# Kernel tuning notes

Hardware: AMD Instinct MI355X
Metric: run time of the kernel (lower is better)

The kernel has to match this reference:

```python
import jax, jax.numpy as jnp
import numpy as np

N, E, F_IN, HID, HEADS, G = 50000, 800000, 128, 32, 8, 64
NEG_SLOPE = 0.2  # PyG GATConv default leaky_relu slope


def gat_conv(x, src, dst, W, att_src, att_dst, bias, heads, out_ch):
    """PyG-style GATConv (concat=True, self-loops already included in src/dst)."""
    n = x.shape[0]
    h = (x @ W).reshape(n, heads, out_ch)            # [N,H,C]
    a_src = jnp.sum(h * att_src, axis=-1)            # [N,H]
    a_dst = jnp.sum(h * att_dst, axis=-1)            # [N,H]
    e = jax.nn.leaky_relu(a_src[src] + a_dst[dst], NEG_SLOPE)  # [Et,H]
    # segment softmax over incoming edges of each destination node
    m = jax.ops.segment_max(e, dst, num_segments=n)
    e = jnp.exp(e - m[dst])
    denom = jax.ops.segment_sum(e, dst, num_segments=n)
    alpha = e / (denom[dst] + 1e-16)                 # [Et,H]
    msg = h[src] * alpha[:, :, None]                 # [Et,H,C]
    out = jax.ops.segment_sum(msg, dst, num_segments=n)
    return out.reshape(n, heads * out_ch) + bias


def setup_inputs() -> dict:
    key = jax.random.key(0)
    ks = jax.random.split(key, 16)
    x = jax.random.normal(ks[0], (N, F_IN), dtype=jnp.float32)
    edge_index = jax.random.randint(ks[1], (2, E), 0, N, dtype=jnp.int64)
    batch = jnp.sort(jax.random.randint(ks[2], (N,), 0, G, dtype=jnp.int64))
    s = 0.05
    params = dict(
        W1=jax.random.normal(ks[3], (F_IN, HEADS * HID), jnp.float32) * s,
        att_src1=jax.random.normal(ks[4], (1, HEADS, HID), jnp.float32) * s,
        att_dst1=jax.random.normal(ks[5], (1, HEADS, HID), jnp.float32) * s,
        b1=jnp.zeros((HEADS * HID,), jnp.float32),
        W2=jax.random.normal(ks[6], (HEADS * HID, HID), jnp.float32) * s,
        att_src2=jax.random.normal(ks[7], (1, 1, HID), jnp.float32) * s,
        att_dst2=jax.random.normal(ks[8], (1, 1, HID), jnp.float32) * s,
        b2=jnp.zeros((HID,), jnp.float32),
        Wo=jax.random.normal(ks[9], (HID, 1), jnp.float32) * s,
        bo=jnp.zeros((1,), jnp.float32),
    )
    return dict(x=x, edge_index=edge_index, batch=batch, **params)


def reference(x, edge_index, batch, W1, att_src1, att_dst1, b1,
              W2, att_src2, att_dst2, b2, Wo, bo):
    # add self loops (PyG GATConv default add_self_loops=True)
    loop = jnp.arange(N, dtype=edge_index.dtype)
    src = jnp.concatenate([edge_index[0], loop])
    dst = jnp.concatenate([edge_index[1], loop])

    h = jax.nn.elu(gat_conv(x, src, dst, W1, att_src1, att_dst1, b1, HEADS, HID))
    # dropout p=0.2 is identity in eval mode
    h = jax.nn.elu(gat_conv(h, src, dst, W2, att_src2, att_dst2, b2, 1, HID))

    # global mean pool over graphs
    sums = jax.ops.segment_sum(h, batch, num_segments=G)          # [G,HID]
    cnts = jax.ops.segment_sum(jnp.ones((N,), h.dtype), batch, num_segments=G)
    pooled = sums / jnp.maximum(cnts, 1.0)[:, None]

    return jax.nn.sigmoid(pooled @ Wo + bo)                        # [G,1]
```

## Files before the change

kernel.cpp:

```cpp
#include <hip/hip_runtime.h>
#include <hip/hip_bf16.h>
#include <math.h>

#define NN 50000
#define NE 800000
#define ET (NE + NN)
#define FIN 128
#define HEADS 8
#define HID 32
#define C1 (HEADS * HID)
#define NG 64
#define NEG 0.2f

#define EPB 4096
#define NBKT 782
#define CAP 2048

typedef __attribute__((ext_vector_type(8))) unsigned short ushort8_t;
typedef __attribute__((ext_vector_type(4))) unsigned short ushort4_t;
typedef __attribute__((ext_vector_type(2))) float float2_t;
typedef __attribute__((ext_vector_type(8))) short bf16x8;
typedef __attribute__((ext_vector_type(4))) float f32x4;

__device__ __forceinline__ float lrelu(float v) { return v > 0.f ? v : NEG * v; }
__device__ __forceinline__ float elu1(float v)  { return v > 0.f ? v : expm1f(v); }
__device__ __forceinline__ unsigned short f2bf(float f) {
    __hip_bfloat16 b = __float2bfloat16(f);
    return *reinterpret_cast<unsigned short*>(&b);
}
__device__ __forceinline__ float bf2f(unsigned short u) {
    return __uint_as_float(((unsigned)u) << 16);
}
__device__ __forceinline__ void dec_fma16(uint4 r, float e, float2_t* acc) {
    float2_t ev = {e, e};
    acc[0] += ev * __builtin_amdgcn_cvt_pk_f32_fp8((int)r.x, false);
    acc[1] += ev * __builtin_amdgcn_cvt_pk_f32_fp8((int)r.x, true);
    acc[2] += ev * __builtin_amdgcn_cvt_pk_f32_fp8((int)r.y, false);
    acc[3] += ev * __builtin_amdgcn_cvt_pk_f32_fp8((int)r.y, true);
    acc[4] += ev * __builtin_amdgcn_cvt_pk_f32_fp8((int)r.z, false);
    acc[5] += ev * __builtin_amdgcn_cvt_pk_f32_fp8((int)r.z, true);
    acc[6] += ev * __builtin_amdgcn_cvt_pk_f32_fp8((int)r.w, false);
    acc[7] += ev * __builtin_amdgcn_cvt_pk_f32_fp8((int)r.w, true);
}

__global__ __launch_bounds__(256) void bkt_scatter_kernel(const int* __restrict__ ei,
                                                          int* __restrict__ bcur,
                                                          unsigned* __restrict__ bkt) {
    __shared__ unsigned ep[EPB];
    __shared__ int lh[NBKT];
    int t = threadIdx.x;
    int base = blockIdx.x * EPB;
    int nloc = ET - base; if (nloc > EPB) nloc = EPB;
    for (int i = t; i < NBKT; i += 256) lh[i] = 0;
    __syncthreads();
    for (int k = t; k < nloc; k += 256) {
        int i = base + k;
        int s, d;
        if (i < NE) { s = ei[i]; d = ei[NE + i]; }
        else        { s = i - NE; d = s; }
        ep[k] = (unsigned)s | ((unsigned)(d & 63) << 16) | ((unsigned)(d >> 6) << 22);
        atomicAdd(&lh[d >> 6], 1);
    }
    __syncthreads();
    for (int i = t; i < NBKT; i += 256) {
        int c = lh[i];
        lh[i] = c ? atomicAdd(&bcur[i], c) : 0;
    }
    __syncthreads();
    for (int k = t; k < nloc; k += 256) {
        unsigned v = ep[k];
        int b = (int)(v >> 22);
        int pos = atomicAdd(&lh[b], 1);
        if (pos < CAP) bkt[(size_t)b * CAP + pos] = v & 0x3FFFFFu;
    }
}

__global__ __launch_bounds__(256) void csr_kernel(const unsigned* __restrict__ bkt,
                                                  const int* __restrict__ bcur,
                                                  int* __restrict__ rowptr,
                                                  int* __restrict__ ssrc) {
    __shared__ int nb[64];
    __shared__ int nc[64];
    __shared__ int red[256];
    int b = blockIdx.x, t = threadIdx.x;
    int partial = 0;
    for (int i = t; i < b; i += 256) partial += bcur[i];
    red[t] = partial;
    if (t < 64) nc[t] = 0;
    __syncthreads();
    if (t < 128) red[t] += red[t + 128];
    __syncthreads();
    if (t < 64) {
        int v = red[t] + red[t + 64];
        #pragma unroll
        for (int off = 32; off; off >>= 1) v += __shfl_down(v, off, 64);
        if (t == 0) red[0] = v;
    }
    __syncthreads();
    int gbase = red[0];
    int cnt = bcur[b]; if (cnt > CAP) cnt = CAP;
    const unsigned* e = bkt + (size_t)b * CAP;
    for (int k = t; k < cnt; k += 256)
        atomicAdd(&nc[e[k] >> 16], 1);
    __syncthreads();
    if (t < 64) {
        int v = nc[t];
        int inc = v;
        #pragma unroll
        for (int off = 1; off < 64; off <<= 1) {
            int u = __shfl_up(inc, off, 64);
            if (t >= off) inc += u;
        }
        int start = gbase + inc - v;
        nb[t] = start;
        int node = b * 64 + t;
        if (node < NN) rowptr[node] = start;
    }
    if (b == NBKT - 1 && t == 0) rowptr[NN] = gbase + cnt;
    __syncthreads();
    for (int k = t; k < cnt; k += 256) {
        unsigned v = e[k];
        int pos = atomicAdd(&nb[v >> 16], 1);
        ssrc[pos] = (int)(v & 0xFFFFu);
    }
}

__global__ __launch_bounds__(256) void cvt_w_kernel(const float* __restrict__ W1,
                                                    const float* __restrict__ W2,
                                                    unsigned short* __restrict__ w1swz,
                                                    unsigned short* __restrict__ w2swz) {
    int bid = blockIdx.x;
    if (bid < 16) {
        int t = bid * 256 + threadIdx.x;
        int fid = t >> 6, lane = t & 63;
        int tnt = fid >> 2, ks = fid & 3;
        int n = tnt * 16 + (lane & 15);
        int k0 = ks * 32 + (lane >> 4) * 8;
        ushort8_t o;
        #pragma unroll
        for (int j = 0; j < 8; ++j) o[j] = f2bf(W1[(k0 + j) * C1 + n]);
        *(ushort8_t*)&w1swz[(size_t)(fid * 64 + lane) * 8] = o;
    } else {
        int t = (bid - 16) * 256 + threadIdx.x;
        int fid = t >> 6, lane = t & 63;
        int nt = fid >> 3, ks = fid & 7;
        int n = nt * 16 + (lane & 15);
        int k0 = ks * 32 + (lane >> 4) * 8;
        ushort8_t o;
        #pragma unroll
        for (int j = 0; j < 8; ++j) o[j] = f2bf(W2[(k0 + j) * HID + n]);
        *(ushort8_t*)&w2swz[(size_t)(fid * 64 + lane) * 8] = o;
    }
}

__global__ __launch_bounds__(256) void gemm1_kernel(
        const float* __restrict__ x, const unsigned short* __restrict__ w1swz,
        const float* __restrict__ attS, const float* __restrict__ attD,
        unsigned char* __restrict__ h1f8, float* __restrict__ aS, float* __restrict__ aD) {
    __shared__ float lds[4 * 16 * 132];
    int t = threadIdx.x, w = t >> 6, lane = t & 63;
    int mh = w & 1, nh = w >> 1;
    int m0 = blockIdx.x * 64 + mh * 32;
    int l15 = lane & 15, l4 = lane >> 4;

    f32x4 acc[2][8];
    #pragma unroll
    for (int mt = 0; mt < 2; ++mt)
        #pragma unroll
        for (int nt = 0; nt < 8; ++nt)
            acc[mt][nt] = (f32x4){0.f, 0.f, 0.f, 0.f};

    int ra = m0 + l15;       if (ra >= NN) ra = NN - 1;
    int rb = m0 + 16 + l15;  if (rb >= NN) rb = NN - 1;
    const float* a0p = x + (size_t)ra * FIN + l4 * 8;
    const float* a1p = x + (size_t)rb * FIN + l4 * 8;

    #pragma unroll
    for (int ks = 0; ks < 4; ++ks) {
        float4 f00 = *(const float4*)(a0p + ks * 32);
        float4 f01 = *(const float4*)(a0p + ks * 32 + 4);
        float4 f10 = *(const float4*)(a1p + ks * 32);
        float4 f11 = *(const float4*)(a1p + ks * 32 + 4);
        bf16x8 af0, af1;
        af0[0] = (short)f2bf(f00.x); af0[1] = (short)f2bf(f00.y);
        af0[2] = (short)f2bf(f00.z); af0[3] = (short)f2bf(f00.w);
        af0[4] = (short)f2bf(f01.x); af0[5] = (short)f2bf(f01.y);
        af0[6] = (short)f2bf(f01.z); af0[7] = (short)f2bf(f01.w);
        af1[0] = (short)f2bf(f10.x); af1[1] = (short)f2bf(f10.y);
        af1[2] = (short)f2bf(f10.z); af1[3] = (short)f2bf(f10.w);
        af1[4] = (short)f2bf(f11.x); af1[5] = (short)f2bf(f11.y);
        af1[6] = (short)f2bf(f11.z); af1[7] = (short)f2bf(f11.w);
        #pragma unroll
        for (int nt = 0; nt < 8; ++nt) {
            bf16x8 bf = *(const bf16x8*)&w1swz[(size_t)(((nh * 8 + nt) * 4 + ks) * 64 + lane) * 8];
            acc[0][nt] = __builtin_amdgcn_mfma_f32_16x16x32_bf16(af0, bf, acc[0][nt], 0, 0, 0);
            acc[1][nt] = __builtin_amdgcn_mfma_f32_16x16x32_bf16(af1, bf, acc[1][nt], 0, 0, 0);
        }
    }

    float* wl = lds + w * 16 * 132;
    #pragma unroll
    for (int mt = 0; mt < 2; ++mt) {
        __syncthreads();
        #pragma unroll
        for (int nt = 0; nt < 8; ++nt)
            #pragma unroll
            for (int r = 0; r < 4; ++r)
                wl[(l4 * 4 + r) * 132 + nt * 16 + l15] = acc[mt][nt][r];
        __syncthreads();
        int row_g = m0 + mt * 16 + l15;
        int cch = l4;
        float v[32];
        #pragma unroll
        for (int i = 0; i < 8; ++i) {
            float4 f = *(const float4*)&wl[l15 * 132 + cch * 32 + i * 4];
            v[i * 4 + 0] = f.x; v[i * 4 + 1] = f.y; v[i * 4 + 2] = f.z; v[i * 4 + 3] = f.w;
        }
        if (row_g < NN) {
            unsigned pk[8];
            #pragma unroll
            for (int i = 0; i < 8; ++i) {
                int p = __builtin_amdgcn_cvt_pk_fp8_f32(v[i * 4 + 0], v[i * 4 + 1], 0, false);
                p = __builtin_amdgcn_cvt_pk_fp8_f32(v[i * 4 + 2], v[i * 4 + 3], p, true);
                pk[i] = (unsigned)p;
            }
            size_t base = (size_t)row_g * C1 + nh * 128 + cch * 32;
            *(uint4*)&h1f8[base]      = make_uint4(pk[0], pk[1], pk[2], pk[3]);
            *(uint4*)&h1f8[base + 16] = make_uint4(pk[4], pk[5], pk[6], pk[7]);
            int h = nh * 4 + cch;
            float ps = 0.f, pd = 0.f;
            #pragma unroll
            for (int i = 0; i < 32; ++i) {
                ps += v[i] * attS[h * 32 + i];
                pd += v[i] * attD[h * 32 + i];
            }
            aS[row_g * HEADS + h] = ps;
            aD[row_g * HEADS + h] = pd;
        }
    }
}

__global__ __launch_bounds__(256) void agg1_kernel(
        const int* __restrict__ rowptr, const int* __restrict__ ssrc,
        const float* __restrict__ aS, const float* __restrict__ aD,
        const unsigned char* __restrict__ h1f8, const float* __restrict__ b1,
        unsigned short* __restrict__ z1b) {
    int d = (blockIdx.x * 256 + threadIdx.x) >> 6;
    int lane = threadIdx.x & 63;
    if (d >= NN) return;
    int start = rowptr[d], end = rowptr[d + 1];
    int q = lane >> 4, sl = lane & 15;
    int h = sl >> 1;
    float adh = aD[d * HEADS + h];
    float2_t acc[8];
    #pragma unroll
    for (int i = 0; i < 8; ++i) acc[i] = (float2_t){0.f, 0.f};
    float den = 0.f;
    int j = start + q;
    for (; j + 12 < end; j += 16) {
        int s0 = ssrc[j], s1 = ssrc[j + 4], s2 = ssrc[j + 8], s3 = ssrc[j + 12];
        uint4 r0 = *(const uint4*)&h1f8[(size_t)s0 * C1 + sl * 16];
        uint4 r1 = *(const uint4*)&h1f8[(size_t)s1 * C1 + sl * 16];
        uint4 r2 = *(const uint4*)&h1f8[(size_t)s2 * C1 + sl * 16];
        uint4 r3 = *(const uint4*)&h1f8[(size_t)s3 * C1 + sl * 16];
        float e0 = __expf(lrelu(aS[s0 * HEADS + h] + adh));
        float e1 = __expf(lrelu(aS[s1 * HEADS + h] + adh));
        float e2 = __expf(lrelu(aS[s2 * HEADS + h] + adh));
        float e3 = __expf(lrelu(aS[s3 * HEADS + h] + adh));
        den += e0 + e1 + e2 + e3;
        dec_fma16(r0, e0, acc);
        dec_fma16(r1, e1, acc);
        dec_fma16(r2, e2, acc);
        dec_fma16(r3, e3, acc);
    }
    for (; j < end; j += 4) {
        int s = ssrc[j];
        uint4 r = *(const uint4*)&h1f8[(size_t)s * C1 + sl * 16];
        float e = __expf(lrelu(aS[s * HEADS + h] + adh));
        den += e;
        dec_fma16(r, e, acc);
    }
    den += __shfl_xor(den, 16, 64);
    den += __shfl_xor(den, 32, 64);
    #pragma unroll
    for (int i = 0; i < 8; ++i) {
        acc[i].x += __shfl_xor(acc[i].x, 16, 64);
        acc[i].y += __shfl_xor(acc[i].y, 16, 64);
        acc[i].x += __shfl_xor(acc[i].x, 32, 64);
        acc[i].y += __shfl_xor(acc[i].y, 32, 64);
    }
    float invd = 1.f / (den + 1e-16f);
    int cb = sl * 16 + q * 4;
    float4 bb = *(const float4*)&b1[cb];
    ushort4_t o;
    o[0] = f2bf(elu1(acc[q * 2 + 0].x * invd + bb.x));
    o[1] = f2bf(elu1(acc[q * 2 + 0].y * invd + bb.y));
    o[2] = f2bf(elu1(acc[q * 2 + 1].x * invd + bb.z));
    o[3] = f2bf(elu1(acc[q * 2 + 1].y * invd + bb.w));
    *(ushort4_t*)&z1b[(size_t)d * C1 + cb] = o;
}

__global__ __launch_bounds__(256) void gemm2_kernel(
        const unsigned short* __restrict__ z1b, const unsigned short* __restrict__ w2swz,
        const float* __restrict__ attS, const float* __restrict__ attD,
        unsigned short* __restrict__ h2b, float* __restrict__ aS2, float* __restrict__ aD2) {
    __shared__ float lds[4 * 16 * 36];
    int t = threadIdx.x, w = t >> 6, lane = t & 63;
    int m0 = blockIdx.x * 64 + w * 16;
    int l15 = lane & 15, l4 = lane >> 4;

    f32x4 acc[2];
    acc[0] = (f32x4){0.f, 0.f, 0.f, 0.f};
    acc[1] = (f32x4){0.f, 0.f, 0.f, 0.f};

    int ra = m0 + l15; if (ra >= NN) ra = NN - 1;
    const unsigned short* ap = z1b + (size_t)ra * C1 + l4 * 8;

    #pragma unroll
    for (int ks = 0; ks < 8; ++ks) {
        bf16x8 af = *(const bf16x8*)(ap + ks * 32);
        #pragma unroll
        for (int nt = 0; nt < 2; ++nt) {
            bf16x8 bf = *(const bf16x8*)&w2swz[(size_t)((nt * 8 + ks) * 64 + lane) * 8];
            acc[nt] = __builtin_amdgcn_mfma_f32_16x16x32_bf16(af, bf, acc[nt], 0, 0, 0);
        }
    }
    float* wl = lds + w * 16 * 36;
    #pragma unroll
    for (int nt = 0; nt < 2; ++nt)
        #pragma unroll
        for (int r = 0; r < 4; ++r)
            wl[(l4 * 4 + r) * 36 + nt * 16 + l15] = acc[nt][r];
    __syncthreads();
    int row_g = m0 + l15;
    float v[8];
    {
        float4 f0 = *(const float4*)&wl[l15 * 36 + l4 * 8];
        float4 f1 = *(const float4*)&wl[l15 * 36 + l4 * 8 + 4];
        v[0] = f0.x; v[1] = f0.y; v[2] = f0.z; v[3] = f0.w;
        v[4] = f1.x; v[5] = f1.y; v[6] = f1.z; v[7] = f1.w;
    }
    float ps = 0.f, pd = 0.f;
    #pragma unroll
    for (int i = 0; i < 8; ++i) {
        ps += v[i] * attS[l4 * 8 + i];
        pd += v[i] * attD[l4 * 8 + i];
    }
    ps += __shfl_xor(ps, 16, 64); ps += __shfl_xor(ps, 32, 64);
    pd += __shfl_xor(pd, 16, 64); pd += __shfl_xor(pd, 32, 64);
    if (row_g < NN) {
        ushort8_t o;
        #pragma unroll
        for (int i = 0; i < 8; ++i) o[i] = f2bf(v[i]);
        *(ushort8_t*)&h2b[(size_t)row_g * HID + l4 * 8] = o;
        if (l4 == 0) { aS2[row_g] = ps; aD2[row_g] = pd; }
    }
}

__global__ __launch_bounds__(256) void agg2_kernel(
        const int* __restrict__ rowptr, const int* __restrict__ ssrc,
        const float* __restrict__ aS, const float* __restrict__ aD,
        const unsigned short* __restrict__ h2b, const float* __restrict__ b2,
        float* __restrict__ z2) {
    int d = (blockIdx.x * 256 + threadIdx.x) >> 6;
    int lane = threadIdx.x & 63;
    if (d >= NN) return;
    int start = rowptr[d], end = rowptr[d + 1];
    int q = lane >> 4, sl = lane & 15;
    float adv = aD[d];
    float2_t a = {0.f, 0.f};
    float den = 0.f;
    int j = start + q;
    for (; j + 12 < end; j += 16) {
        int s0 = ssrc[j], s1 = ssrc[j + 4], s2 = ssrc[j + 8], s3 = ssrc[j + 12];
        unsigned r0 = *(const unsigned*)&h2b[(size_t)s0 * HID + sl * 2];
        unsigned r1 = *(const unsigned*)&h2b[(size_t)s1 * HID + sl * 2];
        unsigned r2 = *(const unsigned*)&h2b[(size_t)s2 * HID + sl * 2];
        unsigned r3 = *(const unsigned*)&h2b[(size_t)s3 * HID + sl * 2];
        float e0 = __expf(lrelu(aS[s0] + adv));
        float e1 = __expf(lrelu(aS[s1] + adv));
        float e2 = __expf(lrelu(aS[s2] + adv));
        float e3 = __expf(lrelu(aS[s3] + adv));
        den += e0 + e1 + e2 + e3;
        a += (float2_t){e0, e0} * (float2_t){bf2f((unsigned short)(r0 & 0xffff)), bf2f((unsigned short)(r0 >> 16))};
        a += (float2_t){e1, e1} * (float2_t){bf2f((unsigned short)(r1 & 0xffff)), bf2f((unsigned short)(r1 >> 16))};
        a += (float2_t){e2, e2} * (float2_t){bf2f((unsigned short)(r2 & 0xffff)), bf2f((unsigned short)(r2 >> 16))};
        a += (float2_t){e3, e3} * (float2_t){bf2f((unsigned short)(r3 & 0xffff)), bf2f((unsigned short)(r3 >> 16))};
    }
    for (; j < end; j += 4) {
        int s = ssrc[j];
        unsigned r = *(const unsigned*)&h2b[(size_t)s * HID + sl * 2];
        float e = __expf(lrelu(aS[s] + adv));
        den += e;
        a += (float2_t){e, e} * (float2_t){bf2f((unsigned short)(r & 0xffff)), bf2f((unsigned short)(r >> 16))};
    }
    den += __shfl_xor(den, 16, 64);
    den += __shfl_xor(den, 32, 64);
    a.x += __shfl_xor(a.x, 16, 64); a.x += __shfl_xor(a.x, 32, 64);
    a.y += __shfl_xor(a.y, 16, 64); a.y += __shfl_xor(a.y, 32, 64);
    if (q == 0) {
        float invd = 1.f / (den + 1e-16f);
        float2 o;
        o.x = elu1(a.x * invd + b2[sl * 2]);
        o.y = elu1(a.y * invd + b2[sl * 2 + 1]);
        *(float2*)&z2[(size_t)d * HID + sl * 2] = o;
    }
}

__global__ __launch_bounds__(256) void pool_kernel(
        const float* __restrict__ z2, const int* __restrict__ batch,
        const float* __restrict__ Wo, const float* __restrict__ bo,
        float* __restrict__ out) {
    __shared__ float sm[256];
    int g = blockIdx.x;
    int t = threadIdx.x;
    int lo = 0, hi = NN;
    while (lo < hi) { int m = (lo + hi) >> 1; if (batch[m] < g) lo = m + 1; else hi = m; }
    int start = lo;
    hi = NN;
    while (lo < hi) { int m = (lo + hi) >> 1; if (batch[m] < g + 1) lo = m + 1; else hi = m; }
    int end = lo;
    int c = t & 31, r = t >> 5;
    float acc = 0.f;
    for (int n = start + r; n < end; n += 8)
        acc += z2[(size_t)n * HID + c];
    sm[t] = acc;
    __syncthreads();
    if (t < 32) {
        float s = 0.f;
        #pragma unroll
        for (int i = 0; i < 8; ++i) s += sm[t + 32 * i];
        float cntf = fmaxf((float)(end - start), 1.f);
        float part = (s / cntf) * Wo[t];
        #pragma unroll
        for (int off = 16; off; off >>= 1) part += __shfl_xor(part, off, 32);
        if (t == 0) out[g] = 1.f / (1.f + __expf(-(part + bo[0])));
    }
}

extern "C" void kernel_launch(void* const* d_in, const int* in_sizes, int n_in,
                              void* d_out, int out_size, void* d_ws, size_t ws_size,
                              hipStream_t stream) {
    const float* x     = (const float*)d_in[0];
    const int*   ei    = (const int*)d_in[1];
    const int*   batch = (const int*)d_in[2];
    const float* W1    = (const float*)d_in[3];
    const float* attS1 = (const float*)d_in[4];
    const float* attD1 = (const float*)d_in[5];
    const float* b1    = (const float*)d_in[6];
    const float* W2    = (const float*)d_in[7];
    const float* attS2 = (const float*)d_in[8];
    const float* attD2 = (const float*)d_in[9];
    const float* b2    = (const float*)d_in[10];
    const float* Wo    = (const float*)d_in[11];
    const float* bo    = (const float*)d_in[12];
    float* out = (float*)d_out;

    char* p = (char*)d_ws;
    auto alloc = [&](size_t bytes) {
        char* r = p;
        p += (bytes + 255) & ~(size_t)255;
        return (void*)r;
    };
    unsigned char*  h1f8  = (unsigned char*)alloc((size_t)NN * C1);
    unsigned short* w1swz = (unsigned short*)alloc((size_t)FIN * C1 * 2);
    unsigned short* w2swz = (unsigned short*)alloc((size_t)C1 * HID * 2);
    unsigned short* z1b   = (unsigned short*)alloc((size_t)NN * C1 * 2);
    unsigned short* h2b   = (unsigned short*)alloc((size_t)NN * HID * 2);
    float* aS1    = (float*)alloc((size_t)NN * HEADS * 4);
    float* aD1    = (float*)alloc((size_t)NN * HEADS * 4);
    float* z2     = (float*)alloc((size_t)NN * HID * 4);
    float* aS2    = (float*)alloc((size_t)NN * 4);
    float* aD2    = (float*)alloc((size_t)NN * 4);
    int*   rowptr = (int*)alloc((size_t)(NN + 1) * 4);
    int*   ssrc   = (int*)alloc((size_t)ET * 4);
    unsigned* bkt = (unsigned*)alloc((size_t)NBKT * CAP * 4);
    int*   bcur   = (int*)alloc((size_t)NBKT * 4);

    hipMemsetAsync(bcur, 0, (size_t)NBKT * 4, stream);
    bkt_scatter_kernel<<<(ET + EPB - 1) / EPB, 256, 0, stream>>>(ei, bcur, bkt);
    csr_kernel<<<NBKT, 256, 0, stream>>>(bkt, bcur, rowptr, ssrc);
    cvt_w_kernel<<<20, 256, 0, stream>>>(W1, W2, w1swz, w2swz);
    gemm1_kernel<<<(NN + 63) / 64, 256, 0, stream>>>(x, w1swz, attS1, attD1, h1f8, aS1, aD1);
    agg1_kernel<<<(NN * 64) / 256, 256, 0, stream>>>(rowptr, ssrc, aS1, aD1, h1f8, b1, z1b);
    gemm2_kernel<<<(NN + 63) / 64, 256, 0, stream>>>(z1b, w2swz, attS2, attD2, h2b, aS2, aD2);
    agg2_kernel<<<(NN * 64 + 255) / 256, 256, 0, stream>>>(rowptr, ssrc, aS2, aD2, h2b, b2, z2);
    pool_kernel<<<NG, 256, 0, stream>>>(z2, batch, Wo, bo, out);
}
```

Measured before the change: 271.8 us.

## Fuse edge bucket scatter with first GEMM in one launch; shrink aggregation unroll

The bucket scatter and the layer-1 GEMM are independent, so they now run as one launch with block-index dispatch over a shared LDS buffer. The weight conversion moves ahead of that launch. This removes one launch and lets the memory-bound atomic scatter overlap with the GEMM blocks. Separately, both aggregation kernels unroll by 2 edges per lane instead of 4, which lowers register pressure but also exposes less memory-level parallelism per thread.

New measurement: 246.6 us. -9.2%, faster.

```diff
diff --git a/kernel.cpp b/kernel.cpp
--- a/kernel.cpp
+++ b/kernel.cpp
@@ -13,6 +13,8 @@
 #define NEG 0.2f
 
 #define EPB 4096
+#define NB_SCAT 208
+#define NB_G1 782
 #define NBKT 782
 #define CAP 2048
 
@@ -43,13 +45,12 @@
     acc[7] += ev * __builtin_amdgcn_cvt_pk_f32_fp8((int)r.w, true);
 }
 
-__global__ __launch_bounds__(256) void bkt_scatter_kernel(const int* __restrict__ ei,
-                                                          int* __restrict__ bcur,
-                                                          unsigned* __restrict__ bkt) {
-    __shared__ unsigned ep[EPB];
-    __shared__ int lh[NBKT];
+__device__ void bkt_scatter_body(char* smem, const int* __restrict__ ei,
+                                 int* __restrict__ bcur, unsigned* __restrict__ bkt, int bid) {
+    unsigned* ep = (unsigned*)smem;
+    int* lh = (int*)(smem + EPB * 4);
     int t = threadIdx.x;
-    int base = blockIdx.x * EPB;
+    int base = bid * EPB;
     int nloc = ET - base; if (nloc > EPB) nloc = EPB;
     for (int i = t; i < NBKT; i += 256) lh[i] = 0;
     __syncthreads();
@@ -75,92 +76,15 @@
     }
 }
 
-__global__ __launch_bounds__(256) void csr_kernel(const unsigned* __restrict__ bkt,
-                                                  const int* __restrict__ bcur,
-                                                  int* __restrict__ rowptr,
-                                                  int* __restrict__ ssrc) {
-    __shared__ int nb[64];
-    __shared__ int nc[64];
-    __shared__ int red[256];
-    int b = blockIdx.x, t = threadIdx.x;
-    int partial = 0;
-    for (int i = t; i < b; i += 256) partial += bcur[i];
-    red[t] = partial;
-    if (t < 64) nc[t] = 0;
-    __syncthreads();
-    if (t < 128) red[t] += red[t + 128];
-    __syncthreads();
-    if (t < 64) {
-        int v = red[t] + red[t + 64];
-        #pragma unroll
-        for (int off = 32; off; off >>= 1) v += __shfl_down(v, off, 64);
-        if (t == 0) red[0] = v;
-    }
-    __syncthreads();
-    int gbase = red[0];
-    int cnt = bcur[b]; if (cnt > CAP) cnt = CAP;
-    const unsigned* e = bkt + (size_t)b * CAP;
-    for (int k = t; k < cnt; k += 256)
-        atomicAdd(&nc[e[k] >> 16], 1);
-    __syncthreads();
-    if (t < 64) {
-        int v = nc[t];
-        int inc = v;
-        #pragma unroll
-        for (int off = 1; off < 64; off <<= 1) {
-            int u = __shfl_up(inc, off, 64);
-            if (t >= off) inc += u;
-        }
-        int start = gbase + inc - v;
-        nb[t] = start;
-        int node = b * 64 + t;
-        if (node < NN) rowptr[node] = start;
-    }
-    if (b == NBKT - 1 && t == 0) rowptr[NN] = gbase + cnt;
-    __syncthreads();
-    for (int k = t; k < cnt; k += 256) {
-        unsigned v = e[k];
-        int pos = atomicAdd(&nb[v >> 16], 1);
-        ssrc[pos] = (int)(v & 0xFFFFu);
-    }
-}
-
-__global__ __launch_bounds__(256) void cvt_w_kernel(const float* __restrict__ W1,
-                                                    const float* __restrict__ W2,
-                                                    unsigned short* __restrict__ w1swz,
-                                                    unsigned short* __restrict__ w2swz) {
-    int bid = blockIdx.x;
-    if (bid < 16) {
-        int t = bid * 256 + threadIdx.x;
-        int fid = t >> 6, lane = t & 63;
-        int tnt = fid >> 2, ks = fid & 3;
-        int n = tnt * 16 + (lane & 15);
-        int k0 = ks * 32 + (lane >> 4) * 8;
-        ushort8_t o;
-        #pragma unroll
-        for (int j = 0; j < 8; ++j) o[j] = f2bf(W1[(k0 + j) * C1 + n]);
-        *(ushort8_t*)&w1swz[(size_t)(fid * 64 + lane) * 8] = o;
-    } else {
-        int t = (bid - 16) * 256 + threadIdx.x;
-        int fid = t >> 6, lane = t & 63;
-        int nt = fid >> 3, ks = fid & 7;
-        int n = nt * 16 + (lane & 15);
-        int k0 = ks * 32 + (lane >> 4) * 8;
-        ushort8_t o;
-        #pragma unroll
-        for (int j = 0; j < 8; ++j) o[j] = f2bf(W2[(k0 + j) * HID + n]);
-        *(ushort8_t*)&w2swz[(size_t)(fid * 64 + lane) * 8] = o;
-    }
-}
-
-__global__ __launch_bounds__(256) void gemm1_kernel(
-        const float* __restrict__ x, const unsigned short* __restrict__ w1swz,
-        const float* __restrict__ attS, const float* __restrict__ attD,
-        unsigned char* __restrict__ h1f8, float* __restrict__ aS, float* __restrict__ aD) {
-    __shared__ float lds[4 * 16 * 132];
+__device__ void gemm1_body(char* smem, const float* __restrict__ x,
+                           const unsigned short* __restrict__ w1swz,
+                           const float* __restrict__ attS, const float* __restrict__ attD,
+                           unsigned char* __restrict__ h1f8, float* __restrict__ aS,
+                           float* __restrict__ aD, int bid) {
+    float* lds = (float*)smem;
     int t = threadIdx.x, w = t >> 6, lane = t & 63;
     int mh = w & 1, nh = w >> 1;
-    int m0 = blockIdx.x * 64 + mh * 32;
+    int m0 = bid * 64 + mh * 32;
     int l15 = lane & 15, l4 = lane >> 4;
 
     f32x4 acc[2][8];
@@ -240,6 +164,96 @@
     }
 }
 
+__global__ __launch_bounds__(256) void fused_front_kernel(
+        const int* __restrict__ ei, int* __restrict__ bcur, unsigned* __restrict__ bkt,
+        const float* __restrict__ x, const unsigned short* __restrict__ w1swz,
+        const float* __restrict__ attS, const float* __restrict__ attD,
+        unsigned char* __restrict__ h1f8, float* __restrict__ aS, float* __restrict__ aD) {
+    __shared__ __align__(16) char smem[33792];
+    if (blockIdx.x < NB_SCAT)
+        bkt_scatter_body(smem, ei, bcur, bkt, blockIdx.x);
+    else
+        gemm1_body(smem, x, w1swz, attS, attD, h1f8, aS, aD, blockIdx.x - NB_SCAT);
+}
+
+__global__ __launch_bounds__(256) void csr_kernel(const unsigned* __restrict__ bkt,
+                                                  const int* __restrict__ bcur,
+                                                  int* __restrict__ rowptr,
+                                                  int* __restrict__ ssrc) {
+    __shared__ int nb[64];
+    __shared__ int nc[64];
+    __shared__ int red[256];
+    int b = blockIdx.x, t = threadIdx.x;
+    int partial = 0;
+    for (int i = t; i < b; i += 256) partial += bcur[i];
+    red[t] = partial;
+    if (t < 64) nc[t] = 0;
+    __syncthreads();
+    if (t < 128) red[t] += red[t + 128];
+    __syncthreads();
+    if (t < 64) {
+        int v = red[t] + red[t + 64];
+        #pragma unroll
+        for (int off = 32; off; off >>= 1) v += __shfl_down(v, off, 64);
+        if (t == 0) red[0] = v;
+    }
+    __syncthreads();
+    int gbase = red[0];
+    int cnt = bcur[b]; if (cnt > CAP) cnt = CAP;
+    const unsigned* e = bkt + (size_t)b * CAP;
+    for (int k = t; k < cnt; k += 256)
+        atomicAdd(&nc[e[k] >> 16], 1);
+    __syncthreads();
+    if (t < 64) {
+        int v = nc[t];
+        int inc = v;
+        #pragma unroll
+        for (int off = 1; off < 64; off <<= 1) {
+            int u = __shfl_up(inc, off, 64);
+            if (t >= off) inc += u;
+        }
+        int start = gbase + inc - v;
+        nb[t] = start;
+        int node = b * 64 + t;
+        if (node < NN) rowptr[node] = start;
+    }
+    if (b == NBKT - 1 && t == 0) rowptr[NN] = gbase + cnt;
+    __syncthreads();
+    for (int k = t; k < cnt; k += 256) {
+        unsigned v = e[k];
+        int pos = atomicAdd(&nb[v >> 16], 1);
+        ssrc[pos] = (int)(v & 0xFFFFu);
+    }
+}
+
+__global__ __launch_bounds__(256) void cvt_w_kernel(const float* __restrict__ W1,
+                                                    const float* __restrict__ W2,
+                                                    unsigned short* __restrict__ w1swz,
+                                                    unsigned short* __restrict__ w2swz) {
+    int bid = blockIdx.x;
+    if (bid < 16) {
+        int t = bid * 256 + threadIdx.x;
+        int fid = t >> 6, lane = t & 63;
+        int tnt = fid >> 2, ks = fid & 3;
+        int n = tnt * 16 + (lane & 15);
+        int k0 = ks * 32 + (lane >> 4) * 8;
+        ushort8_t o;
+        #pragma unroll
+        for (int j = 0; j < 8; ++j) o[j] = f2bf(W1[(k0 + j) * C1 + n]);
+        *(ushort8_t*)&w1swz[(size_t)(fid * 64 + lane) * 8] = o;
+    } else {
+        int t = (bid - 16) * 256 + threadIdx.x;
+        int fid = t >> 6, lane = t & 63;
+        int nt = fid >> 3, ks = fid & 7;
+        int n = nt * 16 + (lane & 15);
+        int k0 = ks * 32 + (lane >> 4) * 8;
+        ushort8_t o;
+        #pragma unroll
+        for (int j = 0; j < 8; ++j) o[j] = f2bf(W2[(k0 + j) * HID + n]);
+        *(ushort8_t*)&w2swz[(size_t)(fid * 64 + lane) * 8] = o;
+    }
+}
+
 __global__ __launch_bounds__(256) void agg1_kernel(
         const int* __restrict__ rowptr, const int* __restrict__ ssrc,
         const float* __restrict__ aS, const float* __restrict__ aD,
@@ -257,21 +271,15 @@
     for (int i = 0; i < 8; ++i) acc[i] = (float2_t){0.f, 0.f};
     float den = 0.f;
     int j = start + q;
-    for (; j + 12 < end; j += 16) {
-        int s0 = ssrc[j], s1 = ssrc[j + 4], s2 = ssrc[j + 8], s3 = ssrc[j + 12];
+    for (; j + 4 < end; j += 8) {
+        int s0 = ssrc[j], s1 = ssrc[j + 4];
         uint4 r0 = *(const uint4*)&h1f8[(size_t)s0 * C1 + sl * 16];
         uint4 r1 = *(const uint4*)&h1f8[(size_t)s1 * C1 + sl * 16];
-        uint4 r2 = *(const uint4*)&h1f8[(size_t)s2 * C1 + sl * 16];
-        uint4 r3 = *(const uint4*)&h1f8[(size_t)s3 * C1 + sl * 16];
         float e0 = __expf(lrelu(aS[s0 * HEADS + h] + adh));
         float e1 = __expf(lrelu(aS[s1 * HEADS + h] + adh));
-        float e2 = __expf(lrelu(aS[s2 * HEADS + h] + adh));
-        float e3 = __expf(lrelu(aS[s3 * HEADS + h] + adh));
-        den += e0 + e1 + e2 + e3;
+        den += e0 + e1;
         dec_fma16(r0, e0, acc);
         dec_fma16(r1, e1, acc);
-        dec_fma16(r2, e2, acc);
-        dec_fma16(r3, e3, acc);
     }
     for (; j < end; j += 4) {
         int s = ssrc[j];
@@ -371,21 +379,15 @@
     float2_t a = {0.f, 0.f};
     float den = 0.f;
     int j = start + q;
-    for (; j + 12 < end; j += 16) {
-        int s0 = ssrc[j], s1 = ssrc[j + 4], s2 = ssrc[j + 8], s3 = ssrc[j + 12];
+    for (; j + 4 < end; j += 8) {
+        int s0 = ssrc[j], s1 = ssrc[j + 4];
         unsigned r0 = *(const unsigned*)&h2b[(size_t)s0 * HID + sl * 2];
         unsigned r1 = *(const unsigned*)&h2b[(size_t)s1 * HID + sl * 2];
-        unsigned r2 = *(const unsigned*)&h2b[(size_t)s2 * HID + sl * 2];
-        unsigned r3 = *(const unsigned*)&h2b[(size_t)s3 * HID + sl * 2];
         float e0 = __expf(lrelu(aS[s0] + adv));
         float e1 = __expf(lrelu(aS[s1] + adv));
-        float e2 = __expf(lrelu(aS[s2] + adv));
-        float e3 = __expf(lrelu(aS[s3] + adv));
-        den += e0 + e1 + e2 + e3;
+        den += e0 + e1;
         a += (float2_t){e0, e0} * (float2_t){bf2f((unsigned short)(r0 & 0xffff)), bf2f((unsigned short)(r0 >> 16))};
         a += (float2_t){e1, e1} * (float2_t){bf2f((unsigned short)(r1 & 0xffff)), bf2f((unsigned short)(r1 >> 16))};
-        a += (float2_t){e2, e2} * (float2_t){bf2f((unsigned short)(r2 & 0xffff)), bf2f((unsigned short)(r2 >> 16))};
-        a += (float2_t){e3, e3} * (float2_t){bf2f((unsigned short)(r3 & 0xffff)), bf2f((unsigned short)(r3 >> 16))};
     }
     for (; j < end; j += 4) {
         int s = ssrc[j];
@@ -478,10 +480,10 @@
     int*   bcur   = (int*)alloc((size_t)NBKT * 4);
 
     hipMemsetAsync(bcur, 0, (size_t)NBKT * 4, stream);
-    bkt_scatter_kernel<<<(ET + EPB - 1) / EPB, 256, 0, stream>>>(ei, bcur, bkt);
+    cvt_w_kernel<<<20, 256, 0, stream>>>(W1, W2, w1swz, w2swz);
+    fused_front_kernel<<<NB_SCAT + NB_G1, 256, 0, stream>>>(
+        ei, bcur, bkt, x, w1swz, attS1, attD1, h1f8, aS1, aD1);
     csr_kernel<<<NBKT, 256, 0, stream>>>(bkt, bcur, rowptr, ssrc);
-    cvt_w_kernel<<<20, 256, 0, stream>>>(W1, W2, w1swz, w2swz);
-    gemm1_kernel<<<(NN + 63) / 64, 256, 0, stream>>>(x, w1swz, attS1, attD1, h1f8, aS1, aD1);
     agg1_kernel<<<(NN * 64) / 256, 256, 0, stream>>>(rowptr, ssrc, aS1, aD1, h1f8, b1, z1b);
     gemm2_kernel<<<(NN + 63) / 64, 256, 0, stream>>>(z1b, w2swz, attS2, attD2, h2b, aS2, aD2);
     agg2_kernel<<<(NN * 64 + 255) / 256, 256, 0, stream>>>(rowptr, ssrc, aS2, aD2, h2b, b2, z2);
```

## Fuse CSR construction into aggregation kernels via per-block shared-memory sort

Applied to the files above, without the earlier changes.

Removes the separate csr_kernel pass that built rowptr/ssrc in global memory. Each aggregation block now reads its 64-node bucket, counts and sorts the edges for its 16 destination nodes in shared memory, then aggregates 4 nodes per wave. This saves a kernel launch and the global CSR write and read. In exchange, each bucket is read and filtered four times per aggregation kernel, so the sort is redone in both agg1 and agg2, and the inner loop unroll drops from 4 to 2. The shared sort buffer is capped at 768 edges per 16 nodes, which could silently drop edges on skewed graphs.

Result: faster. 253.8 us (-6.6%).

```diff
diff --git a/kernel.cpp b/kernel.cpp
--- a/kernel.cpp
+++ b/kernel.cpp
@@ -15,6 +15,7 @@
 #define EPB 4096
 #define NBKT 782
 #define CAP 2048
+#define CAPP 768
 
 typedef __attribute__((ext_vector_type(8))) unsigned short ushort8_t;
 typedef __attribute__((ext_vector_type(4))) unsigned short ushort4_t;
@@ -72,56 +73,6 @@
         int b = (int)(v >> 22);
         int pos = atomicAdd(&lh[b], 1);
         if (pos < CAP) bkt[(size_t)b * CAP + pos] = v & 0x3FFFFFu;
-    }
-}
-
-__global__ __launch_bounds__(256) void csr_kernel(const unsigned* __restrict__ bkt,
-                                                  const int* __restrict__ bcur,
-                                                  int* __restrict__ rowptr,
-                                                  int* __restrict__ ssrc) {
-    __shared__ int nb[64];
-    __shared__ int nc[64];
-    __shared__ int red[256];
-    int b = blockIdx.x, t = threadIdx.x;
-    int partial = 0;
-    for (int i = t; i < b; i += 256) partial += bcur[i];
-    red[t] = partial;
-    if (t < 64) nc[t] = 0;
-    __syncthreads();
-    if (t < 128) red[t] += red[t + 128];
-    __syncthreads();
-    if (t < 64) {
-        int v = red[t] + red[t + 64];
-        #pragma unroll
-        for (int off = 32; off; off >>= 1) v += __shfl_down(v, off, 64);
-        if (t == 0) red[0] = v;
-    }
-    __syncthreads();
-    int gbase = red[0];
-    int cnt = bcur[b]; if (cnt > CAP) cnt = CAP;
-    const unsigned* e = bkt + (size_t)b * CAP;
-    for (int k = t; k < cnt; k += 256)
-        atomicAdd(&nc[e[k] >> 16], 1);
-    __syncthreads();
-    if (t < 64) {
-        int v = nc[t];
-        int inc = v;
-        #pragma unroll
-        for (int off = 1; off < 64; off <<= 1) {
-            int u = __shfl_up(inc, off, 64);
-            if (t >= off) inc += u;
-        }
-        int start = gbase + inc - v;
-        nb[t] = start;
-        int node = b * 64 + t;
-        if (node < NN) rowptr[node] = start;
-    }
-    if (b == NBKT - 1 && t == 0) rowptr[NN] = gbase + cnt;
-    __syncthreads();
-    for (int k = t; k < cnt; k += 256) {
-        unsigned v = e[k];
-        int pos = atomicAdd(&nb[v >> 16], 1);
-        ssrc[pos] = (int)(v & 0xFFFFu);
     }
 }
 
@@ -241,63 +192,97 @@
 }
 
 __global__ __launch_bounds__(256) void agg1_kernel(
-        const int* __restrict__ rowptr, const int* __restrict__ ssrc,
+        const unsigned* __restrict__ bkt, const int* __restrict__ bcur,
         const float* __restrict__ aS, const float* __restrict__ aD,
         const unsigned char* __restrict__ h1f8, const float* __restrict__ b1,
         unsigned short* __restrict__ z1b) {
-    int d = (blockIdx.x * 256 + threadIdx.x) >> 6;
-    int lane = threadIdx.x & 63;
-    if (d >= NN) return;
-    int start = rowptr[d], end = rowptr[d + 1];
+    __shared__ unsigned short srt[CAPP];
+    __shared__ int cnt_s[16], base_s[16], cur_s[16];
+    int bid = blockIdx.x;
+    int b = bid >> 2, part = bid & 3;
+    int t = threadIdx.x;
+    int cnt = bcur[b]; if (cnt > CAP) cnt = CAP;
+    if (t < 16) cnt_s[t] = 0;
+    __syncthreads();
+    const unsigned* e = bkt + (size_t)b * CAP;
+    int dlo = part * 16;
+    for (int k = t; k < cnt; k += 256) {
+        int dl = (int)(e[k] >> 16) - dlo;
+        if ((unsigned)dl < 16u) atomicAdd(&cnt_s[dl], 1);
+    }
+    __syncthreads();
+    if (t < 16) {
+        int v = cnt_s[t];
+        int inc = v;
+        #pragma unroll
+        for (int off = 1; off < 16; off <<= 1) {
+            int u = __shfl_up(inc, off, 64);
+            if (t >= off) inc += u;
+        }
+        base_s[t] = inc - v;
+        cur_s[t] = inc - v;
+    }
+    __syncthreads();
+    for (int k = t; k < cnt; k += 256) {
+        unsigned v = e[k];
+        int dl = (int)(v >> 16) - dlo;
+        if ((unsigned)dl < 16u) {
+            int pos = atomicAdd(&cur_s[dl], 1);
+            if (pos < CAPP) srt[pos] = (unsigned short)(v & 0xFFFFu);
+        }
+    }
+    __syncthreads();
+    int wv = t >> 6, lane = t & 63;
     int q = lane >> 4, sl = lane & 15;
     int h = sl >> 1;
-    float adh = aD[d * HEADS + h];
-    float2_t acc[8];
-    #pragma unroll
-    for (int i = 0; i < 8; ++i) acc[i] = (float2_t){0.f, 0.f};
-    float den = 0.f;
-    int j = start + q;
-    for (; j + 12 < end; j += 16) {
-        int s0 = ssrc[j], s1 = ssrc[j + 4], s2 = ssrc[j + 8], s3 = ssrc[j + 12];
-        uint4 r0 = *(const uint4*)&h1f8[(size_t)s0 * C1 + sl * 16];
-        uint4 r1 = *(const uint4*)&h1f8[(size_t)s1 * C1 + sl * 16];
-        uint4 r2 = *(const uint4*)&h1f8[(size_t)s2 * C1 + sl * 16];
-        uint4 r3 = *(const uint4*)&h1f8[(size_t)s3 * C1 + sl * 16];
-        float e0 = __expf(lrelu(aS[s0 * HEADS + h] + adh));
-        float e1 = __expf(lrelu(aS[s1 * HEADS + h] + adh));
-        float e2 = __expf(lrelu(aS[s2 * HEADS + h] + adh));
-        float e3 = __expf(lrelu(aS[s3 * HEADS + h] + adh));
-        den += e0 + e1 + e2 + e3;
-        dec_fma16(r0, e0, acc);
-        dec_fma16(r1, e1, acc);
-        dec_fma16(r2, e2, acc);
-        dec_fma16(r3, e3, acc);
-    }
-    for (; j < end; j += 4) {
-        int s = ssrc[j];
-        uint4 r = *(const uint4*)&h1f8[(size_t)s * C1 + sl * 16];
-        float e = __expf(lrelu(aS[s * HEADS + h] + adh));
-        den += e;
-        dec_fma16(r, e, acc);
-    }
-    den += __shfl_xor(den, 16, 64);
-    den += __shfl_xor(den, 32, 64);
-    #pragma unroll
-    for (int i = 0; i < 8; ++i) {
-        acc[i].x += __shfl_xor(acc[i].x, 16, 64);
-        acc[i].y += __shfl_xor(acc[i].y, 16, 64);
-        acc[i].x += __shfl_xor(acc[i].x, 32, 64);
-        acc[i].y += __shfl_xor(acc[i].y, 32, 64);
-    }
-    float invd = 1.f / (den + 1e-16f);
-    int cb = sl * 16 + q * 4;
-    float4 bb = *(const float4*)&b1[cb];
-    ushort4_t o;
-    o[0] = f2bf(elu1(acc[q * 2 + 0].x * invd + bb.x));
-    o[1] = f2bf(elu1(acc[q * 2 + 0].y * invd + bb.y));
-    o[2] = f2bf(elu1(acc[q * 2 + 1].x * invd + bb.z));
-    o[3] = f2bf(elu1(acc[q * 2 + 1].y * invd + bb.w));
-    *(ushort4_t*)&z1b[(size_t)d * C1 + cb] = o;
+    #pragma unroll
+    for (int i = 0; i < 4; ++i) {
+        int dl = wv * 4 + i;
+        int d = b * 64 + dlo + dl;
+        if (d >= NN) continue;
+        int start = base_s[dl], end = start + cnt_s[dl];
+        float adh = aD[d * HEADS + h];
+        float2_t acc[8];
+        #pragma unroll
+        for (int i2 = 0; i2 < 8; ++i2) acc[i2] = (float2_t){0.f, 0.f};
+        float den = 0.f;
+        int j = start + q;
+        for (; j + 4 < end; j += 8) {
+            int s0 = srt[j], s1 = srt[j + 4];
+            uint4 r0 = *(const uint4*)&h1f8[(size_t)s0 * C1 + sl * 16];
+            uint4 r1 = *(const uint4*)&h1f8[(size_t)s1 * C1 + sl * 16];
+            float e0 = __expf(lrelu(aS[s0 * HEADS + h] + adh));
+            float e1 = __expf(lrelu(aS[s1 * HEADS + h] + adh));
+            den += e0 + e1;
+            dec_fma16(r0, e0, acc);
+            dec_fma16(r1, e1, acc);
+        }
+        for (; j < end; j += 4) {
+            int s = srt[j];
+            uint4 r = *(const uint4*)&h1f8[(size_t)s * C1 + sl * 16];
+            float ee = __expf(lrelu(aS[s * HEADS + h] + adh));
+            den += ee;
+            dec_fma16(r, ee, acc);
+        }
+        den += __shfl_xor(den, 16, 64);
+        den += __shfl_xor(den, 32, 64);
+        #pragma unroll
+        for (int i2 = 0; i2 < 8; ++i2) {
+            acc[i2].x += __shfl_xor(acc[i2].x, 16, 64);
+            acc[i2].y += __shfl_xor(acc[i2].y, 16, 64);
+            acc[i2].x += __shfl_xor(acc[i2].x, 32, 64);
+            acc[i2].y += __shfl_xor(acc[i2].y, 32, 64);
+        }
+        float invd = 1.f / (den + 1e-16f);
+        int cb = sl * 16 + q * 4;
+        float4 bb = *(const float4*)&b1[cb];
+        ushort4_t o;
+        o[0] = f2bf(elu1(acc[q * 2 + 0].x * invd + bb.x));
+        o[1] = f2bf(elu1(acc[q * 2 + 0].y * invd + bb.y));
+        o[2] = f2bf(elu1(acc[q * 2 + 1].x * invd + bb.z));
+        o[3] = f2bf(elu1(acc[q * 2 + 1].y * invd + bb.w));
+        *(ushort4_t*)&z1b[(size_t)d * C1 + cb] = o;
+    }
 }
 
 __global__ __launch_bounds__(256) void gemm2_kernel(
@@ -358,52 +343,86 @@
 }
 
 __global__ __launch_bounds__(256) void agg2_kernel(
-        const int* __restrict__ rowptr, const int* __restrict__ ssrc,
+        const unsigned* __restrict__ bkt, const int* __restrict__ bcur,
         const float* __restrict__ aS, const float* __restrict__ aD,
         const unsigned short* __restrict__ h2b, const float* __restrict__ b2,
         float* __restrict__ z2) {
-    int d = (blockIdx.x * 256 + threadIdx.x) >> 6;
-    int lane = threadIdx.x & 63;
-    if (d >= NN) return;
-    int start = rowptr[d], end = rowptr[d + 1];
+    __shared__ unsigned short srt[CAPP];
+    __shared__ int cnt_s[16], base_s[16], cur_s[16];
+    int bid = blockIdx.x;
+    int b = bid >> 2, part = bid & 3;
+    int t = threadIdx.x;
+    int cnt = bcur[b]; if (cnt > CAP) cnt = CAP;
+    if (t < 16) cnt_s[t] = 0;
+    __syncthreads();
+    const unsigned* e = bkt + (size_t)b * CAP;
+    int dlo = part * 16;
+    for (int k = t; k < cnt; k += 256) {
+        int dl = (int)(e[k] >> 16) - dlo;
+        if ((unsigned)dl < 16u) atomicAdd(&cnt_s[dl], 1);
+    }
+    __syncthreads();
+    if (t < 16) {
+        int v = cnt_s[t];
+        int inc = v;
+        #pragma unroll
+        for (int off = 1; off < 16; off <<= 1) {
+            int u = __shfl_up(inc, off, 64);
+            if (t >= off) inc += u;
+        }
+        base_s[t] = inc - v;
+        cur_s[t] = inc - v;
+    }
+    __syncthreads();
+    for (int k = t; k < cnt; k += 256) {
+        unsigned v = e[k];
+        int dl = (int)(v >> 16) - dlo;
+        if ((unsigned)dl < 16u) {
+            int pos = atomicAdd(&cur_s[dl], 1);
+            if (pos < CAPP) srt[pos] = (unsigned short)(v & 0xFFFFu);
+        }
+    }
+    __syncthreads();
+    int wv = t >> 6, lane = t & 63;
     int q = lane >> 4, sl = lane & 15;
-    float adv = aD[d];
-    float2_t a = {0.f, 0.f};
-    float den = 0.f;
-    int j = start + q;
-    for (; j + 12 < end; j += 16) {
-        int s0 = ssrc[j], s1 = ssrc[j + 4], s2 = ssrc[j + 8], s3 = ssrc[j + 12];
-        unsigned r0 = *(const unsigned*)&h2b[(size_t)s0 * HID + sl * 2];
-        unsigned r1 = *(const unsigned*)&h2b[(size_t)s1 * HID + sl * 2];
-        unsigned r2 = *(const unsigned*)&h2b[(size_t)s2 * HID + sl * 2];
-        unsigned r3 = *(const unsigned*)&h2b[(size_t)s3 * HID + sl * 2];
-        float e0 = __expf(lrelu(aS[s0] + adv));
-        float e1 = __expf(lrelu(aS[s1] + adv));
-        float e2 = __expf(lrelu(aS[s2] + adv));
-        float e3 = __expf(lrelu(aS[s3] + adv));
-        den += e0 + e1 + e2 + e3;
-        a += (float2_t){e0, e0} * (float2_t){bf2f((unsigned short)(r0 & 0xffff)), bf2f((unsigned short)(r0 >> 16))};
-        a += (float2_t){e1, e1} * (float2_t){bf2f((unsigned short)(r1 & 0xffff)), bf2f((unsigned short)(r1 >> 16))};
-        a += (float2_t){e2, e2} * (float2_t){bf2f((unsigned short)(r2 & 0xffff)), bf2f((unsigned short)(r2 >> 16))};
-        a += (float2_t){e3, e3} * (float2_t){bf2f((unsigned short)(r3 & 0xffff)), bf2f((unsigned short)(r3 >> 16))};
-    }
-    for (; j < end; j += 4) {
-        int s = ssrc[j];
-        unsigned r = *(const unsigned*)&h2b[(size_t)s * HID + sl * 2];
-        float e = __expf(lrelu(aS[s] + adv));
-        den += e;
-        a += (float2_t){e, e} * (float2_t){bf2f((unsigned short)(r & 0xffff)), bf2f((unsigned short)(r >> 16))};
-    }
-    den += __shfl_xor(den, 16, 64);
-    den += __shfl_xor(den, 32, 64);
-    a.x += __shfl_xor(a.x, 16, 64); a.x += __shfl_xor(a.x, 32, 64);
-    a.y += __shfl_xor(a.y, 16, 64); a.y += __shfl_xor(a.y, 32, 64);
-    if (q == 0) {
-        float invd = 1.f / (den + 1e-16f);
-        float2 o;
-        o.x = elu1(a.x * invd + b2[sl * 2]);
-        o.y = elu1(a.y * invd + b2[sl * 2 + 1]);
-        *(float2*)&z2[(size_t)d * HID + sl * 2] = o;
+    #pragma unroll
+    for (int i = 0; i < 4; ++i) {
+        int dl = wv * 4 + i;
+        int d = b * 64 + dlo + dl;
+        if (d >= NN) continue;
+        int start = base_s[dl], end = start + cnt_s[dl];
+        float adv = aD[d];
+        float2_t a = {0.f, 0.f};
+        float den = 0.f;
+        int j = start + q;
+        for (; j + 4 < end; j += 8) {
+            int s0 = srt[j], s1 = srt[j + 4];
+            unsigned r0 = *(const unsigned*)&h2b[(size_t)s0 * HID + sl * 2];
+            unsigned r1 = *(const unsigned*)&h2b[(size_t)s1 * HID + sl * 2];
+            float e0 = __expf(lrelu(aS[s0] + adv));
+            float e1 = __expf(lrelu(aS[s1] + adv));
+            den += e0 + e1;
+            a += (float2_t){e0, e0} * (float2_t){bf2f((unsigned short)(r0 & 0xffff)), bf2f((unsigned short)(r0 >> 16))};
+            a += (float2_t){e1, e1} * (float2_t){bf2f((unsigned short)(r1 & 0xffff)), bf2f((unsigned short)(r1 >> 16))};
+        }
+        for (; j < end; j += 4) {
+            int s = srt[j];
+            unsigned r = *(const unsigned*)&h2b[(size_t)s * HID + sl * 2];
+            float ee = __expf(lrelu(aS[s] + adv));
+            den += ee;
+            a += (float2_t){ee, ee} * (float2_t){bf2f((unsigned short)(r & 0xffff)), bf2f((unsigned short)(r >> 16))};
+        }
+        den += __shfl_xor(den, 16, 64);
+        den += __shfl_xor(den, 32, 64);
+        a.x += __shfl_xor(a.x, 16, 64); a.x += __shfl_xor(a.x, 32, 64);
+        a.y += __shfl_xor(a.y, 16, 64); a.y += __shfl_xor(a.y, 32, 64);
+        if (q == 0) {
+            float invd = 1.f / (den + 1e-16f);
+            float2 o;
+            o.x = elu1(a.x * invd + b2[sl * 2]);
+            o.y = elu1(a.y * invd + b2[sl * 2 + 1]);
+            *(float2*)&z2[(size_t)d * HID + sl * 2] = o;
+        }
     }
 }
 
@@ -472,18 +491,15 @@
     float* z2     = (float*)alloc((size_t)NN * HID * 4);
     float* aS2    = (float*)alloc((size_t)NN * 4);
     float* aD2    = (float*)alloc((size_t)NN * 4);
-    int*   rowptr = (int*)alloc((size_t)(NN + 1) * 4);
-    int*   ssrc   = (int*)alloc((size_t)ET * 4);
     unsigned* bkt = (unsigned*)alloc((size_t)NBKT * CAP * 4);
     int*   bcur   = (int*)alloc((size_t)NBKT * 4);
 
     hipMemsetAsync(bcur, 0, (size_t)NBKT * 4, stream);
+    cvt_w_kernel<<<20, 256, 0, stream>>>(W1, W2, w1swz, w2swz);
     bkt_scatter_kernel<<<(ET + EPB - 1) / EPB, 256, 0, stream>>>(ei, bcur, bkt);
-    csr_kernel<<<NBKT, 256, 0, stream>>>(bkt, bcur, rowptr, ssrc);
-    cvt_w_kernel<<<20, 256, 0, stream>>>(W1, W2, w1swz, w2swz);
     gemm1_kernel<<<(NN + 63) / 64, 256, 0, stream>>>(x, w1swz, attS1, attD1, h1f8, aS1, aD1);
-    agg1_kernel<<<(NN * 64) / 256, 256, 0, stream>>>(rowptr, ssrc, aS1, aD1, h1f8, b1, z1b);
+    agg1_kernel<<<NBKT * 4, 256, 0, stream>>>(bkt, bcur, aS1, aD1, h1f8, b1, z1b);
     gemm2_kernel<<<(NN + 63) / 64, 256, 0, stream>>>(z1b, w2swz, attS2, attD2, h2b, aS2, aD2);
-    agg2_kernel<<<(NN * 64 + 255) / 256, 256, 0, stream>>>(rowptr, ssrc, aS2, aD2, h2b, b2, z2);
+    agg2_kernel<<<NBKT * 4, 256, 0, stream>>>(bkt, bcur, aS2, aD2, h2b, b2, z2);
     pool_kernel<<<NG, 256, 0, stream>>>(z2, batch, Wo, bo, out);
 }
```
